# Performance work log

Measured on AMD Instinct MI355X. Metric: run time of the kernel, lower is better.

## Reference

```python
import jax, jax.numpy as jnp
import numpy as np
from jax import lax

B, L, H, E, V = 16, 128, 1024, 512, 32000
MAX_LENGTH = 128
SOS_INDEX = 1
NUM_LAYERS = 2


def setup_inputs() -> dict:
    key = jax.random.key(0)
    ks = jax.random.split(key, 16)
    inp = {}
    inp['input_tensor'] = jax.random.randint(ks[0], (B, L), 0, V)
    inp['target_tensor'] = jax.random.randint(ks[1], (B, L), 0, V)
    inp['true_sample'] = 1
    s = lambda k, shape, fan: jax.random.normal(k, shape, jnp.float32) / np.float32(np.sqrt(fan))
    inp['embedding'] = jax.random.normal(ks[2], (V, E), jnp.float32) * 0.02
    inp['enc_W'] = s(ks[3], (E, H), E)
    inp['enc_b'] = jnp.zeros((H,), jnp.float32)
    inp['Wih0'] = s(ks[4], (E, 3 * H), E)
    inp['Whh0'] = s(ks[5], (H, 3 * H), H)
    inp['bih0'] = jnp.zeros((3 * H,), jnp.float32)
    inp['bhh0'] = jnp.zeros((3 * H,), jnp.float32)
    inp['Wih1'] = s(ks[6], (H, 3 * H), H)
    inp['Whh1'] = s(ks[7], (H, 3 * H), H)
    inp['bih1'] = jnp.zeros((3 * H,), jnp.float32)
    inp['bhh1'] = jnp.zeros((3 * H,), jnp.float32)
    inp['W_out'] = s(ks[8], (2 * H, V), 2 * H)
    inp['b_out'] = jnp.zeros((V,), jnp.float32)
    return inp


def _gru_cell(x, h, Wih, Whh, bih, bhh):
    gx = x @ Wih + bih
    gh = h @ Whh + bhh
    xr, xz, xn = jnp.split(gx, 3, axis=-1)
    hr, hz, hn = jnp.split(gh, 3, axis=-1)
    r = jax.nn.sigmoid(xr + hr)
    z = jax.nn.sigmoid(xz + hz)
    n = jnp.tanh(xn + r * hn)
    return (1.0 - z) * n + z * h


def _forward(input_tensor, true_sample, embedding, enc_W, enc_b,
             Wih0, Whh0, bih0, bhh0, Wih1, Whh1, bih1, bhh1, W_out, b_out):
    batch_size, input_length = input_tensor.shape
    target_length = input_length
    # Encoder: embed + per-timestep projection -> [B, L, H]
    enc_emb = embedding[input_tensor]
    enc_hidden = jnp.tanh(enc_emb @ enc_W + enc_b)
    enc_hidden_t = jnp.transpose(enc_hidden, (1, 0, 2))  # [L, B, H]
    # Pad at the front to max_length (mirrors the copy loop)
    encoder_outputs = jnp.zeros((MAX_LENGTH, batch_size, H), enc_hidden.dtype)
    encoder_outputs = encoder_outputs.at[MAX_LENGTH - input_length:].set(enc_hidden_t)
    # Decoder initial hidden: last encoder state stacked over layers
    h_init = enc_hidden_t[-1]  # [B, H]
    # NOTE: original never updates decoder_input inside the loop -> constant SOS
    x0 = jnp.broadcast_to(embedding[SOS_INDEX], (batch_size, E))
    inv_sqrt_h = np.float32(1.0 / np.sqrt(H))

    def step(carry, _):
        h0, h1 = carry
        h0 = _gru_cell(x0, h0, Wih0, Whh0, bih0, bhh0)
        h1 = _gru_cell(h0, h1, Wih1, Whh1, bih1, bhh1)
        scores = jnp.einsum('bh,lbh->bl', h1, encoder_outputs) * inv_sqrt_h
        attn = jax.nn.softmax(scores, axis=-1)
        ctx = jnp.einsum('bl,lbh->bh', attn, encoder_outputs)
        logits = jnp.concatenate([h1, ctx], axis=-1) @ W_out + b_out
        return (h0, h1), jax.nn.sigmoid(logits)

    _, probs = lax.scan(step, (h_init, h_init), None, length=target_length)
    decoder_outputs = jnp.transpose(probs, (1, 0, 2))  # [B, T, V]
    # Scalar gather: p[b,w] = decoder_outputs[b, w, input_tensor[b, w]]
    out_probabilities = jnp.take_along_axis(decoder_outputs, input_tensor[..., None], axis=2)[..., 0]
    target = jnp.full(input_tensor.shape, np.float32(int(true_sample)), jnp.float32)
    p = jnp.clip(out_probabilities, 1e-12, 1.0 - 1e-7)
    bce = -(target * jnp.log(p) + (1.0 - target) * jnp.log1p(-p))
    loss = jnp.mean(bce) / np.float32(batch_size)
    return loss, out_probabilities


def reference(input_tensor, target_tensor, true_sample, embedding, enc_W, enc_b,
              Wih0, Whh0, bih0, bhh0, Wih1, Whh1, bih1, bhh1, W_out, b_out):
    return _forward(input_tensor, true_sample, embedding, enc_W, enc_b,
                    Wih0, Whh0, bih0, bhh0, Wih1, Whh1, bih1, bhh1, W_out, b_out)
```

## Files before the change

### kernel.cpp

```cpp
#include <hip/hip_runtime.h>
#include <math.h>

#define BB 16
#define LL 128
#define HH 1024
#define EE 512
#define VV 32000
#define G3 3072
#define NBLK 256

__device__ __forceinline__ float sigmoidf_(float x){ return 1.0f/(1.0f+expf(-x)); }

__device__ __forceinline__ float redk(float v){
  v += __shfl_xor(v, 1, 64); v += __shfl_xor(v, 2, 64);
  v += __shfl_xor(v, 4, 64); v += __shfl_xor(v, 8, 64);
  v += __shfl_xor(v, 16, 64);
  return v;
}

__global__ void k_rowidx(const int* __restrict__ inp, int* __restrict__ idx){
  int r = blockIdx.x*256 + threadIdx.x;
  if (r < 2048){ int l = r >> 4, b = r & 15; idx[r] = inp[b*LL + l]; }
}

template<int ACT, int KK>
__global__ __launch_bounds__(256) void k_gemm(const float* __restrict__ A, const int* __restrict__ rowidx,
                       const float* __restrict__ Bm, const float* __restrict__ bias,
                       float* __restrict__ C, int N){
  constexpr int KS = (KK==512)?9:10;
  __shared__ float As[32*KK];
  const int tid = threadIdx.x;
  const int r0 = blockIdx.x*32;
  const int c  = blockIdx.y*512 + (tid<<1);
  for (int i = tid; i < 32*KK; i += 256){
    int rr = i >> KS;
    int row = r0 + rr;
    int arow = rowidx ? rowidx[row] : row;
    int kk = i - (rr<<KS);
    As[i] = A[(size_t)arow*KK + kk];
  }
  __syncthreads();
  float2 acc[32];
  #pragma unroll
  for (int r=0;r<32;r++){ acc[r].x=0.f; acc[r].y=0.f; }
  for (int k=0;k<KK;k++){
    const float2 w = *(const float2*)(Bm + (size_t)k*N + c);
    #pragma unroll
    for (int r=0;r<32;r++){
      float a = As[(r<<KS)+k];
      acc[r].x = fmaf(a,w.x,acc[r].x);
      acc[r].y = fmaf(a,w.y,acc[r].y);
    }
  }
  const float2 bv = *(const float2*)(bias + c);
  #pragma unroll
  for (int r=0;r<32;r++){
    float x = acc[r].x + bv.x, y = acc[r].y + bv.y;
    if (ACT==1){ x = tanhf(x); y = tanhf(y); }
    *(float2*)(C + (size_t)(r0+r)*N + c) = make_float2(x,y);
  }
}

__global__ __launch_bounds__(512,1) void k_chains(
    const float* enclast, float* H0all, float* H1all,
    const float* __restrict__ Whh0, const float* __restrict__ Whh1,
    const float* __restrict__ Wih0, const float* __restrict__ Wih1,
    const float* __restrict__ emb,
    const float* __restrict__ bih0, const float* __restrict__ bhh0,
    const float* __restrict__ bhh1, const float* __restrict__ bih1,
    int* flagsB, int* flagsA)
{
  __shared__ float w0l[12][1024];
  __shared__ float w1l[12][1024];
  __shared__ float wil[12][1024];
  const int tid  = threadIdx.x;
  const int lane = tid & 63;
  const int wv   = tid >> 6;
  const int kl   = lane & 31;
  const int bh   = lane >> 5;
  const int jb   = blockIdx.x << 2;
  const int b    = (wv << 1) + bh;
  const int jp_  = jb + kl;
  const bool act = (kl < 4);
  const int koff = kl << 2;

  float g0r=0.f, g0z=0.f, g0n=0.f;
  {
    for (int idx = tid; idx < 1536; idx += 512){
      int g = idx >> 9, k = idx & 511;
      float4 a = *(const float4*)(Wih0 + (size_t)k*G3 + g*1024 + jb);
      w0l[g*4+0][k]=a.x; w0l[g*4+1][k]=a.y; w0l[g*4+2][k]=a.z; w0l[g*4+3][k]=a.w;
    }
    __syncthreads();
    const float* e1 = emb + EE;
    float ag[12];
    #pragma unroll
    for (int c=0;c<12;c++) ag[c]=0.f;
    #pragma unroll
    for (int i=0;i<4;i++){
      float4 e = *(const float4*)(e1 + i*128 + koff);
      #pragma unroll
      for (int c=0;c<12;c++){
        const float4 w = *(const float4*)(&w0l[c][i*128 + koff]);
        float v = ag[c];
        v=fmaf(w.x,e.x,v); v=fmaf(w.y,e.y,v); v=fmaf(w.z,e.z,v); v=fmaf(w.w,e.w,v);
        ag[c]=v;
      }
    }
    #pragma unroll
    for (int c=0;c<12;c++) ag[c] = redk(ag[c]);
    if (act){
      float sr=0.f, sz=0.f, sn=0.f;
      #pragma unroll
      for (int jj=0;jj<4;jj++){
        bool sel = (kl==jj);
        sr = sel ? ag[jj]   : sr;
        sz = sel ? ag[4+jj] : sz;
        sn = sel ? ag[8+jj] : sn;
      }
      g0r = sr + bih0[jp_];
      g0z = sz + bih0[1024+jp_];
      g0n = sn + bih0[2048+jp_];
    }
    __syncthreads();
  }

  for (int idx = tid; idx < 3072; idx += 512){
    int g = idx >> 10, k = idx & 1023;
    float4 a = *(const float4*)(Whh0 + (size_t)k*G3 + g*1024 + jb);
    w0l[g*4+0][k]=a.x; w0l[g*4+1][k]=a.y; w0l[g*4+2][k]=a.z; w0l[g*4+3][k]=a.w;
    float4 d = *(const float4*)(Whh1 + (size_t)k*G3 + g*1024 + jb);
    w1l[g*4+0][k]=d.x; w1l[g*4+1][k]=d.y; w1l[g*4+2][k]=d.z; w1l[g*4+3][k]=d.w;
    float4 e = *(const float4*)(Wih1 + (size_t)k*G3 + g*1024 + jb);
    wil[g*4+0][k]=e.x; wil[g*4+1][k]=e.y; wil[g*4+2][k]=e.z; wil[g*4+3][k]=e.w;
  }
  float b0r_=0.f,b0z_=0.f,b0n_=0.f,b1r_=0.f,b1z_=0.f,b1n_=0.f,bir_=0.f,biz_=0.f,bin_=0.f;
  if (act){
    b0r_ = bhh0[jp_]; b0z_ = bhh0[1024+jp_]; b0n_ = bhh0[2048+jp_];
    b1r_ = bhh1[jp_]; b1z_ = bhh1[1024+jp_]; b1n_ = bhh1[2048+jp_];
    bir_ = bih1[jp_]; biz_ = bih1[1024+jp_]; bin_ = bih1[2048+jp_];
  }
  __syncthreads();

  const int myflag = (int)blockIdx.x * 32;
  const int pollfl = (tid & 255) * 32;

  for (int t = 0; t <= LL+1; ++t){
    if (t >= 1){
      while (__hip_atomic_load(&flagsB[pollfl], __ATOMIC_RELAXED,
                               __HIP_MEMORY_SCOPE_AGENT) < t)
        __builtin_amdgcn_s_sleep(1);
      __syncthreads();
    }

    if (t >= 2){
      const float* h0row = H0all + (size_t)(t-2)*(BB*HH) + (size_t)b*HH;
      const float* h1row = ((t==2) ? enclast : (H1all + (size_t)(t-3)*(BB*HH)))
                           + (size_t)b*HH;
      float hprev1 = 0.f;
      if (act) hprev1 = h1row[kl];
      if (act) hprev1 = h1row[jp_];
      float accg[12], acc1[12];
      #pragma unroll
      for (int c=0;c<12;c++){ accg[c]=0.f; acc1[c]=0.f; }
      #pragma unroll
      for (int i=0;i<8;i++){
        float4 h0v = *(const float4*)(h0row + i*128 + koff);
        float4 h1v = *(const float4*)(h1row + i*128 + koff);
        #pragma unroll
        for (int c=0;c<12;c++){
          const float4 wg = *(const float4*)(&wil[c][i*128 + koff]);
          float u = accg[c];
          u=fmaf(wg.x,h0v.x,u); u=fmaf(wg.y,h0v.y,u); u=fmaf(wg.z,h0v.z,u); u=fmaf(wg.w,h0v.w,u);
          accg[c]=u;
          const float4 w1 = *(const float4*)(&w1l[c][i*128 + koff]);
          float v = acc1[c];
          v=fmaf(w1.x,h1v.x,v); v=fmaf(w1.y,h1v.y,v); v=fmaf(w1.z,h1v.z,v); v=fmaf(w1.w,h1v.w,v);
          acc1[c]=v;
        }
      }
      #pragma unroll
      for (int c=0;c<12;c++){ accg[c] = redk(accg[c]); acc1[c] = redk(acc1[c]); }
      if (act){
        float ghr=0.f, ghz=0.f, ghn=0.f, gxr=0.f, gxz=0.f, gxn=0.f;
        #pragma unroll
        for (int jj=0;jj<4;jj++){
          bool sel = (kl==jj);
          ghr = sel ? acc1[jj]   : ghr;
          ghz = sel ? acc1[4+jj] : ghz;
          ghn = sel ? acc1[8+jj] : ghn;
          gxr = sel ? accg[jj]   : gxr;
          gxz = sel ? accg[4+jj] : gxz;
          gxn = sel ? accg[8+jj] : gxn;
        }
        float r = sigmoidf_(gxr + bir_ + ghr + b1r_);
        float z = sigmoidf_(gxz + biz_ + ghz + b1z_);
        float n = tanhf    (gxn + bin_ + r*(ghn + b1n_));
        float hnew = (1.f-z)*n + z*hprev1;
        __hip_atomic_store((int*)&H1all[(size_t)(t-2)*(BB*HH) + (size_t)b*HH + jp_],
                           __float_as_int(hnew),
                           __ATOMIC_RELAXED, __HIP_MEMORY_SCOPE_AGENT);
      }
    }

    asm volatile("s_waitcnt vmcnt(0)" ::: "memory");
    __syncthreads();
    if (tid == 0)
      __hip_atomic_store(&flagsB[myflag], t+1,
                         __ATOMIC_RELAXED, __HIP_MEMORY_SCOPE_AGENT);

    if (t >= 1){
      while (__hip_atomic_load(&flagsA[pollfl], __ATOMIC_RELAXED,
                               __HIP_MEMORY_SCOPE_AGENT) < t)
        __builtin_amdgcn_s_sleep(1);
      __syncthreads();
    }

    if (t < LL){
      const float* h0row = ((t==0) ? enclast : (H0all + (size_t)(t-1)*(BB*HH)))
                           + (size_t)b*HH;
      float hprev0 = 0.f;
      if (act) hprev0 = h0row[jp_];
      float acc0[12];
      #pragma unroll
      for (int c=0;c<12;c++) acc0[c]=0.f;
      #pragma unroll
      for (int i=0;i<8;i++){
        float4 hv = *(const float4*)(h0row + i*128 + koff);
        #pragma unroll
        for (int c=0;c<12;c++){
          const float4 w = *(const float4*)(&w0l[c][i*128 + koff]);
          float v = acc0[c];
          v=fmaf(w.x,hv.x,v); v=fmaf(w.y,hv.y,v); v=fmaf(w.z,hv.z,v); v=fmaf(w.w,hv.w,v);
          acc0[c]=v;
        }
      }
      #pragma unroll
      for (int c=0;c<12;c++) acc0[c] = redk(acc0[c]);
      if (act){
        float ghr=0.f, ghz=0.f, ghn=0.f;
        #pragma unroll
        for (int jj=0;jj<4;jj++){
          bool sel = (kl==jj);
          ghr = sel ? acc0[jj]   : ghr;
          ghz = sel ? acc0[4+jj] : ghz;
          ghn = sel ? acc0[8+jj] : ghn;
        }
        float r = sigmoidf_(g0r + ghr + b0r_);
        float z = sigmoidf_(g0z + ghz + b0z_);
        float n = tanhf    (g0n + r*(ghn + b0n_));
        float hnew = (1.f-z)*n + z*hprev0;
        __hip_atomic_store((int*)&H0all[(size_t)t*(BB*HH) + (size_t)b*HH + jp_],
                           __float_as_int(hnew),
                           __ATOMIC_RELAXED, __HIP_MEMORY_SCOPE_AGENT);
      }
    }

    asm volatile("s_waitcnt vmcnt(0)" ::: "memory");
    __syncthreads();
    if (tid == 0)
      __hip_atomic_store(&flagsA[myflag], t+1,
                         __ATOMIC_RELAXED, __HIP_MEMORY_SCOPE_AGENT);
  }
}

__global__ __launch_bounds__(256) void k_attn(const float* __restrict__ enc, const float* __restrict__ H1,
                       float* __restrict__ ctx){
  __shared__ float h1s[8][HH];
  __shared__ float sc[8][LL];
  __shared__ float part[2][8][LL];
  const int tid = threadIdx.x;
  const int s0 = blockIdx.x*8, b = blockIdx.y;
  for (int i = tid; i < 8*HH; i += 256){
    int si = i >> 10, k = i & 1023;
    h1s[si][k] = H1[(size_t)(s0+si)*BB*HH + (size_t)b*HH + k];
  }
  __syncthreads();
  {
    const int l = tid & 127, half = tid >> 7;
    const float4* er = (const float4*)(enc + ((size_t)l*BB + b)*HH + half*512);
    float a[8];
    #pragma unroll
    for (int s=0;s<8;s++) a[s]=0.f;
    for (int q=0;q<128;q++){
      float4 e = er[q];
      #pragma unroll
      for (int s=0;s<8;s++){
        const float4 h = *(const float4*)(&h1s[s][half*512 + q*4]);
        a[s] += h.x*e.x + h.y*e.y + h.z*e.z + h.w*e.w;
      }
    }
    #pragma unroll
    for (int s=0;s<8;s++) part[half][s][l] = a[s];
  }
  __syncthreads();
  for (int p = tid; p < 1024; p += 256){
    int s = p >> 7, l = p & 127;
    sc[s][l] = (part[0][s][l] + part[1][s][l]) * 0.03125f;
  }
  __syncthreads();
  {
    int s = tid >> 5, lid = tid & 31;
    float v0 = sc[s][lid], v1 = sc[s][lid+32], v2 = sc[s][lid+64], v3 = sc[s][lid+96];
    float m = fmaxf(fmaxf(v0,v1),fmaxf(v2,v3));
    for (int off=16; off>=1; off>>=1) m = fmaxf(m, __shfl_xor(m, off, 32));
    float e0=__expf(v0-m), e1=__expf(v1-m), e2=__expf(v2-m), e3=__expf(v3-m);
    float ssum = e0+e1+e2+e3;
    for (int off=16; off>=1; off>>=1) ssum += __shfl_xor(ssum, off, 32);
    float inv = 1.0f/ssum;
    sc[s][lid]=e0*inv; sc[s][lid+32]=e1*inv; sc[s][lid+64]=e2*inv; sc[s][lid+96]=e3*inv;
  }
  __syncthreads();
  {
    float acc[4][8];
    #pragma unroll
    for (int q=0;q<4;q++)
      #pragma unroll
      for (int s=0;s<8;s++) acc[q][s]=0.f;
    for (int l=0;l<128;l++){
      const float* er = enc + ((size_t)l*BB + b)*HH + tid;
      float a[8];
      #pragma unroll
      for (int s=0;s<8;s++) a[s] = sc[s][l];
      #pragma unroll
      for (int q=0;q<4;q++){
        float e = er[q*256];
        #pragma unroll
        for (int s=0;s<8;s++) acc[q][s] = fmaf(a[s], e, acc[q][s]);
      }
    }
    #pragma unroll
    for (int s=0;s<8;s++)
      #pragma unroll
      for (int q=0;q<4;q++)
        ctx[(size_t)(s0+s)*BB*HH + (size_t)b*HH + tid + q*256] = acc[q][s];
  }
}

__global__ __launch_bounds__(256) void k_logit(const float* __restrict__ H1, const float* __restrict__ ctx,
                        const float* __restrict__ Wout, const float* __restrict__ bout,
                        const int* __restrict__ inp, const int* __restrict__ ts,
                        float* __restrict__ outp, float* __restrict__ bce){
  __shared__ float rbuf[256];
  const int i = blockIdx.x;
  const int b = i >> 7, t = i & 127;
  const int v = inp[b*LL + t];
  const int tid = threadIdx.x;
  const float* h1r = H1 + ((size_t)t*BB + b)*HH;
  const float* cxr = ctx + ((size_t)t*BB + b)*HH;
  float acc = 0.f;
  #pragma unroll
  for (int q=0;q<4;q++){
    int k = tid + q*256;
    acc = fmaf(h1r[k], Wout[(size_t)k*VV + v], acc);
  }
  #pragma unroll
  for (int q=0;q<4;q++){
    int k = tid + q*256;
    acc = fmaf(cxr[k], Wout[(size_t)(k+1024)*VV + v], acc);
  }
  rbuf[tid] = acc;
  __syncthreads();
  for (int s=128; s>0; s>>=1){
    if (tid < s) rbuf[tid] += rbuf[tid+s];
    __syncthreads();
  }
  if (tid==0){
    float logit = rbuf[0] + bout[v];
    float p = 1.0f/(1.0f + expf(-logit));
    outp[b*LL + t] = p;
    float pc = fminf(fmaxf(p, 1e-12f), 1.0f - 1e-7f);
    float tg = (float)ts[0];
    bce[i] = -(tg*logf(pc) + (1.0f-tg)*log1pf(-pc));
  }
}

__global__ void k_loss(const float* __restrict__ bce, float* __restrict__ out0){
  __shared__ float rbuf[256];
  int tid = threadIdx.x;
  float s = 0.f;
  for (int i = tid; i < 2048; i += 256) s += bce[i];
  rbuf[tid] = s; __syncthreads();
  for (int st=128; st>0; st>>=1){
    if (tid<st) rbuf[tid]+=rbuf[tid+st];
    __syncthreads();
  }
  if (tid==0) out0[0] = rbuf[0] * (1.0f/(2048.0f*16.0f));
}

extern "C" void kernel_launch(void* const* d_in, const int* in_sizes, int n_in,
                              void* d_out, int out_size, void* d_ws, size_t ws_size,
                              hipStream_t stream){
  (void)in_sizes; (void)n_in; (void)out_size; (void)ws_size;
  const int*   inp   = (const int*)d_in[0];
  const int*   ts    = (const int*)d_in[2];
  const float* emb   = (const float*)d_in[3];
  const float* encW  = (const float*)d_in[4];
  const float* encb  = (const float*)d_in[5];
  const float* Wih0  = (const float*)d_in[6];
  const float* Whh0  = (const float*)d_in[7];
  const float* bih0  = (const float*)d_in[8];
  const float* bhh0  = (const float*)d_in[9];
  const float* Wih1  = (const float*)d_in[10];
  const float* Whh1  = (const float*)d_in[11];
  const float* bih1  = (const float*)d_in[12];
  const float* bhh1  = (const float*)d_in[13];
  const float* Wout  = (const float*)d_in[14];
  const float* bout  = (const float*)d_in[15];
  float* out = (float*)d_out;

  float* ws      = (float*)d_ws;
  float* enc_out = ws;
  float* H0      = enc_out + 2097152;
  float* H1      = H0 + 2097152;
  float* GX1     = H1 + 2097152;
  float* CTX     = GX1 + 6291456;
  float* gx0     = CTX + 2097152;
  float* bceb    = gx0 + 3072;
  int*   rowidx  = (int*)(bceb + 2048);
  int*   flagsB  = rowidx + 2048;
  int*   flagsA  = flagsB + 256*32;

  hipMemsetAsync(flagsB, 0, 512*32*sizeof(int), stream);
  k_rowidx<<<8,256,0,stream>>>(inp, rowidx);
  k_gemm<1,512><<<dim3(64,2),256,0,stream>>>(emb, rowidx, encW, encb, enc_out, HH);

  const float* enclast = enc_out + (size_t)127*BB*HH;

  k_chains<<<NBLK,512,0,stream>>>(enclast, H0, H1, Whh0, Whh1, Wih0, Wih1, emb,
                                  bih0, bhh0, bhh1, bih1, flagsB, flagsA);
  k_attn<<<dim3(16,16),256,0,stream>>>(enc_out, H1, CTX);
  k_logit<<<2048,256,0,stream>>>(H1, CTX, Wout, bout, inp, ts, out+1, bceb);
  k_loss<<<1,256,0,stream>>>(bceb, out);
}
```

Measured before the change: 2.079 ms.

## Re-tile persistent GRU chain kernel to reuse LDS weights across four batch rows

After: 2.089 ms. About the same (+0.5%).

```diff
diff --git a/kernel.cpp b/kernel.cpp
--- a/kernel.cpp
+++ b/kernel.cpp
@@ -11,7 +11,13 @@
 
 __device__ __forceinline__ float sigmoidf_(float x){ return 1.0f/(1.0f+expf(-x)); }
 
-__device__ __forceinline__ float redk(float v){
+__device__ __forceinline__ float red64(float v){
+  v += __shfl_xor(v, 1, 64); v += __shfl_xor(v, 2, 64);
+  v += __shfl_xor(v, 4, 64); v += __shfl_xor(v, 8, 64);
+  v += __shfl_xor(v, 16, 64); v += __shfl_xor(v, 32, 64);
+  return v;
+}
+__device__ __forceinline__ float red32(float v){
   v += __shfl_xor(v, 1, 64); v += __shfl_xor(v, 2, 64);
   v += __shfl_xor(v, 4, 64); v += __shfl_xor(v, 8, 64);
   v += __shfl_xor(v, 16, 64);
@@ -73,16 +79,32 @@
   __shared__ float w0l[12][1024];
   __shared__ float w1l[12][1024];
   __shared__ float wil[12][1024];
+  __shared__ float gxbuf[16*12];
   const int tid  = threadIdx.x;
-  const int lane = tid & 63;
-  const int wv   = tid >> 6;
-  const int kl   = lane & 31;
-  const int bh   = lane >> 5;
   const int jb   = blockIdx.x << 2;
-  const int b    = (wv << 1) + bh;
-  const int jp_  = jb + kl;
-  const bool act = (kl < 4);
-  const int koff = kl << 2;
+  const int waveid = tid >> 6;
+  const int cgA = waveid >> 2;
+  const int bgA = waveid & 3;
+  const int kgA = tid & 63;
+  const int koffA = kgA << 2;
+  const int b0A = bgA << 2;
+  const int cgB = waveid >> 1;
+  const int bgB = ((waveid & 1) << 1) | ((tid >> 5) & 1);
+  const int kgB = tid & 31;
+  const int koffB = kgB << 2;
+  const int b0B = bgB << 2;
+  const int mB  = cgB >> 1;
+
+  const bool pwA = (kgA < 8);
+  const int  jlA = (cgA << 1) + (kgA & 1);
+  const int  jpA = jb + jlA;
+  const int  biA = (kgA >> 1) & 3;
+  const int  bA  = b0A + biA;
+  const bool pwB = (cgB >= 2) && (kgB < 8);
+  const int  jlB = ((cgB & 1) << 1) + (kgB & 1);
+  const int  jpB = jb + jlB;
+  const int  biB = (kgB >> 1) & 3;
+  const int  bB  = b0B + biB;
 
   float g0r=0.f, g0z=0.f, g0n=0.f;
   {
@@ -93,34 +115,28 @@
     }
     __syncthreads();
     const float* e1 = emb + EE;
-    float ag[12];
-    #pragma unroll
-    for (int c=0;c<12;c++) ag[c]=0.f;
-    #pragma unroll
-    for (int i=0;i<4;i++){
-      float4 e = *(const float4*)(e1 + i*128 + koff);
-      #pragma unroll
-      for (int c=0;c<12;c++){
-        const float4 w = *(const float4*)(&w0l[c][i*128 + koff]);
-        float v = ag[c];
+    float ag[6];
+    #pragma unroll
+    for (int cl=0;cl<6;cl++) ag[cl]=0.f;
+    #pragma unroll
+    for (int u=0;u<2;u++){
+      float4 e = *(const float4*)(e1 + u*256 + koffA);
+      #pragma unroll
+      for (int cl=0;cl<6;cl++){
+        const int gc = ((cl>>1)<<2) + (cgA<<1) + (cl&1);
+        const float4 w = *(const float4*)(&w0l[gc][u*256 + koffA]);
+        float v = ag[cl];
         v=fmaf(w.x,e.x,v); v=fmaf(w.y,e.y,v); v=fmaf(w.z,e.z,v); v=fmaf(w.w,e.w,v);
-        ag[c]=v;
-      }
-    }
-    #pragma unroll
-    for (int c=0;c<12;c++) ag[c] = redk(ag[c]);
-    if (act){
-      float sr=0.f, sz=0.f, sn=0.f;
-      #pragma unroll
-      for (int jj=0;jj<4;jj++){
-        bool sel = (kl==jj);
-        sr = sel ? ag[jj]   : sr;
-        sz = sel ? ag[4+jj] : sz;
-        sn = sel ? ag[8+jj] : sn;
-      }
-      g0r = sr + bih0[jp_];
-      g0z = sz + bih0[1024+jp_];
-      g0n = sn + bih0[2048+jp_];
+        ag[cl]=v;
+      }
+    }
+    #pragma unroll
+    for (int cl=0;cl<6;cl++) ag[cl] = red64(ag[cl]);
+    if (pwA){
+      const int jj = kgA & 1;
+      g0r = (jj ? ag[1] : ag[0]) + bih0[jpA];
+      g0z = (jj ? ag[3] : ag[2]) + bih0[1024+jpA];
+      g0n = (jj ? ag[5] : ag[4]) + bih0[2048+jpA];
     }
     __syncthreads();
   }
@@ -134,11 +150,12 @@
     float4 e = *(const float4*)(Wih1 + (size_t)k*G3 + g*1024 + jb);
     wil[g*4+0][k]=e.x; wil[g*4+1][k]=e.y; wil[g*4+2][k]=e.z; wil[g*4+3][k]=e.w;
   }
-  float b0r_=0.f,b0z_=0.f,b0n_=0.f,b1r_=0.f,b1z_=0.f,b1n_=0.f,bir_=0.f,biz_=0.f,bin_=0.f;
-  if (act){
-    b0r_ = bhh0[jp_]; b0z_ = bhh0[1024+jp_]; b0n_ = bhh0[2048+jp_];
-    b1r_ = bhh1[jp_]; b1z_ = bhh1[1024+jp_]; b1n_ = bhh1[2048+jp_];
-    bir_ = bih1[jp_]; biz_ = bih1[1024+jp_]; bin_ = bih1[2048+jp_];
+  float b0rA=0.f,b0zA=0.f,b0nA=0.f;
+  if (pwA){ b0rA = bhh0[jpA]; b0zA = bhh0[1024+jpA]; b0nA = bhh0[2048+jpA]; }
+  float birB=0.f,bizB=0.f,binB=0.f,b1rB=0.f,b1zB=0.f,b1nB=0.f;
+  if (pwB){
+    birB = bih1[jpB]; bizB = bih1[1024+jpB]; binB = bih1[2048+jpB];
+    b1rB = bhh1[jpB]; b1zB = bhh1[1024+jpB]; b1nB = bhh1[2048+jpB];
   }
   __syncthreads();
 
@@ -154,50 +171,75 @@
     }
 
     if (t >= 2){
-      const float* h0row = H0all + (size_t)(t-2)*(BB*HH) + (size_t)b*HH;
-      const float* h1row = ((t==2) ? enclast : (H1all + (size_t)(t-3)*(BB*HH)))
-                           + (size_t)b*HH;
+      const float* hp0 = H0all + (size_t)(t-2)*(BB*HH);
+      const float* hp1 = (t==2) ? enclast : (H1all + (size_t)(t-3)*(BB*HH));
+      const float* hr  = mB ? hp1 : hp0;
       float hprev1 = 0.f;
-      if (act) hprev1 = h1row[kl];
-      if (act) hprev1 = h1row[jp_];
-      float accg[12], acc1[12];
-      #pragma unroll
-      for (int c=0;c<12;c++){ accg[c]=0.f; acc1[c]=0.f; }
-      #pragma unroll
-      for (int i=0;i<8;i++){
-        float4 h0v = *(const float4*)(h0row + i*128 + koff);
-        float4 h1v = *(const float4*)(h1row + i*128 + koff);
-        #pragma unroll
-        for (int c=0;c<12;c++){
-          const float4 wg = *(const float4*)(&wil[c][i*128 + koff]);
-          float u = accg[c];
-          u=fmaf(wg.x,h0v.x,u); u=fmaf(wg.y,h0v.y,u); u=fmaf(wg.z,h0v.z,u); u=fmaf(wg.w,h0v.w,u);
-          accg[c]=u;
-          const float4 w1 = *(const float4*)(&w1l[c][i*128 + koff]);
-          float v = acc1[c];
-          v=fmaf(w1.x,h1v.x,v); v=fmaf(w1.y,h1v.y,v); v=fmaf(w1.z,h1v.z,v); v=fmaf(w1.w,h1v.w,v);
-          acc1[c]=v;
+      if (pwB) hprev1 = hp1[(size_t)bB*HH + jpB];
+
+      float accB[6][4];
+      #pragma unroll
+      for (int cl=0;cl<6;cl++)
+        #pragma unroll
+        for (int bi=0;bi<4;bi++) accB[cl][bi]=0.f;
+
+      #pragma unroll
+      for (int u=0;u<8;u++){
+        float4 h4[4];
+        #pragma unroll
+        for (int bi=0;bi<4;bi++)
+          h4[bi] = *(const float4*)(hr + (size_t)(b0B+bi)*HH + u*128 + koffB);
+        #pragma unroll
+        for (int cl=0;cl<6;cl++){
+          const int gc = ((cl>>1)<<2) + ((cgB&1)<<1) + (cl&1);
+          const float4 w = mB ? *(const float4*)(&w1l[gc][u*128 + koffB])
+                              : *(const float4*)(&wil[gc][u*128 + koffB]);
+          #pragma unroll
+          for (int bi=0;bi<4;bi++){
+            float v = accB[cl][bi];
+            v=fmaf(w.x,h4[bi].x,v); v=fmaf(w.y,h4[bi].y,v);
+            v=fmaf(w.z,h4[bi].z,v); v=fmaf(w.w,h4[bi].w,v);
+            accB[cl][bi]=v;
+          }
         }
       }
       #pragma unroll
-      for (int c=0;c<12;c++){ accg[c] = redk(accg[c]); acc1[c] = redk(acc1[c]); }
-      if (act){
-        float ghr=0.f, ghz=0.f, ghn=0.f, gxr=0.f, gxz=0.f, gxn=0.f;
-        #pragma unroll
-        for (int jj=0;jj<4;jj++){
-          bool sel = (kl==jj);
-          ghr = sel ? acc1[jj]   : ghr;
-          ghz = sel ? acc1[4+jj] : ghz;
-          ghn = sel ? acc1[8+jj] : ghn;
-          gxr = sel ? accg[jj]   : gxr;
-          gxz = sel ? accg[4+jj] : gxz;
-          gxn = sel ? accg[8+jj] : gxn;
+      for (int cl=0;cl<6;cl++)
+        #pragma unroll
+        for (int bi=0;bi<4;bi++) accB[cl][bi] = red32(accB[cl][bi]);
+
+      if (mB == 0){
+        #pragma unroll
+        for (int cl=0;cl<6;cl++){
+          if (kgB == cl){
+            const int g = cl >> 1;
+            const int jl = ((cgB&1)<<1) + (cl&1);
+            #pragma unroll
+            for (int bi=0;bi<4;bi++)
+              gxbuf[(b0B+bi)*12 + g*4 + jl] = accB[cl][bi];
+          }
         }
-        float r = sigmoidf_(gxr + bir_ + ghr + b1r_);
-        float z = sigmoidf_(gxz + biz_ + ghz + b1z_);
-        float n = tanhf    (gxn + bin_ + r*(ghn + b1n_));
+      }
+      __syncthreads();
+      if (pwB){
+        float ghr=0.f, ghz=0.f, ghn=0.f;
+        #pragma unroll
+        for (int jj=0;jj<2;jj++)
+          #pragma unroll
+          for (int ii=0;ii<4;ii++){
+            bool sel = ((kgB&1)==jj) & (biB==ii);
+            ghr = sel ? accB[jj][ii]   : ghr;
+            ghz = sel ? accB[2+jj][ii] : ghz;
+            ghn = sel ? accB[4+jj][ii] : ghn;
+          }
+        float gxr = gxbuf[bB*12 + 0*4 + jlB];
+        float gxz = gxbuf[bB*12 + 1*4 + jlB];
+        float gxn = gxbuf[bB*12 + 2*4 + jlB];
+        float r = sigmoidf_(gxr + birB + ghr + b1rB);
+        float z = sigmoidf_(gxz + bizB + ghz + b1zB);
+        float n = tanhf    (gxn + binB + r*(ghn + b1nB));
         float hnew = (1.f-z)*n + z*hprev1;
-        __hip_atomic_store((int*)&H1all[(size_t)(t-2)*(BB*HH) + (size_t)b*HH + jp_],
+        __hip_atomic_store((int*)&H1all[(size_t)(t-2)*(BB*HH) + (size_t)bB*HH + jpB],
                            __float_as_int(hnew),
                            __ATOMIC_RELAXED, __HIP_MEMORY_SCOPE_AGENT);
       }
@@ -217,40 +259,56 @@
     }
 
     if (t < LL){
-      const float* h0row = ((t==0) ? enclast : (H0all + (size_t)(t-1)*(BB*HH)))
-                           + (size_t)b*HH;
+      const float* hp0 = (t==0) ? enclast : (H0all + (size_t)(t-1)*(BB*HH));
       float hprev0 = 0.f;
-      if (act) hprev0 = h0row[jp_];
-      float acc0[12];
-      #pragma unroll
-      for (int c=0;c<12;c++) acc0[c]=0.f;
-      #pragma unroll
-      for (int i=0;i<8;i++){
-        float4 hv = *(const float4*)(h0row + i*128 + koff);
-        #pragma unroll
-        for (int c=0;c<12;c++){
-          const float4 w = *(const float4*)(&w0l[c][i*128 + koff]);
-          float v = acc0[c];
-          v=fmaf(w.x,hv.x,v); v=fmaf(w.y,hv.y,v); v=fmaf(w.z,hv.z,v); v=fmaf(w.w,hv.w,v);
-          acc0[c]=v;
+      if (pwA) hprev0 = hp0[(size_t)bA*HH + jpA];
+
+      float acc0[6][4];
+      #pragma unroll
+      for (int cl=0;cl<6;cl++)
+        #pragma unroll
+        for (int bi=0;bi<4;bi++) acc0[cl][bi]=0.f;
+
+      #pragma unroll
+      for (int u=0;u<4;u++){
+        float4 h4[4];
+        #pragma unroll
+        for (int bi=0;bi<4;bi++)
+          h4[bi] = *(const float4*)(hp0 + (size_t)(b0A+bi)*HH + u*256 + koffA);
+        #pragma unroll
+        for (int cl=0;cl<6;cl++){
+          const int gc = ((cl>>1)<<2) + (cgA<<1) + (cl&1);
+          const float4 w = *(const float4*)(&w0l[gc][u*256 + koffA]);
+          #pragma unroll
+          for (int bi=0;bi<4;bi++){
+            float v = acc0[cl][bi];
+            v=fmaf(w.x,h4[bi].x,v); v=fmaf(w.y,h4[bi].y,v);
+            v=fmaf(w.z,h4[bi].z,v); v=fmaf(w.w,h4[bi].w,v);
+            acc0[cl][bi]=v;
+          }
         }
       }
       #pragma unroll
-      for (int c=0;c<12;c++) acc0[c] = redk(acc0[c]);
-      if (act){
+      for (int cl=0;cl<6;cl++)
+        #pragma unroll
+        for (int bi=0;bi<4;bi++) acc0[cl][bi] = red64(acc0[cl][bi]);
+
+      if (pwA){
         float ghr=0.f, ghz=0.f, ghn=0.f;
         #pragma unroll
-        for (int jj=0;jj<4;jj++){
-          bool sel = (kl==jj);
-          ghr = sel ? acc0[jj]   : ghr;
-          ghz = sel ? acc0[4+jj] : ghz;
-          ghn = sel ? acc0[8+jj] : ghn;
-        }
-        float r = sigmoidf_(g0r + ghr + b0r_);
-        float z = sigmoidf_(g0z + ghz + b0z_);
-        float n = tanhf    (g0n + r*(ghn + b0n_));
+        for (int jj=0;jj<2;jj++)
+          #pragma unroll
+          for (int ii=0;ii<4;ii++){
+            bool sel = ((kgA&1)==jj) & (biA==ii);
+            ghr = sel ? acc0[jj][ii]   : ghr;
+            ghz = sel ? acc0[2+jj][ii] : ghz;
+            ghn = sel ? acc0[4+jj][ii] : ghn;
+          }
+        float r = sigmoidf_(g0r + ghr + b0rA);
+        float z = sigmoidf_(g0z + ghz + b0zA);
+        float n = tanhf    (g0n + r*(ghn + b0nA));
         float hnew = (1.f-z)*n + z*hprev0;
-        __hip_atomic_store((int*)&H0all[(size_t)t*(BB*HH) + (size_t)b*HH + jp_],
+        __hip_atomic_store((int*)&H0all[(size_t)t*(BB*HH) + (size_t)bA*HH + jpA],
                            __float_as_int(hnew),
                            __ATOMIC_RELAXED, __HIP_MEMORY_SCOPE_AGENT);
       }
```
